# Optimization experiments

Measured on AMD Instinct MI355X. Metric: run time of the kernel, lower is better.

Reference implementation:

```python
import jax, jax.numpy as jnp
import numpy as np

B, N = 32, 1024  # batch, square grid size (Ny == Nx forced by expand_as in the torch module)


def setup_inputs() -> dict:
    key = jax.random.key(0)
    k1, k2, k3 = jax.random.split(key, 3)
    xaxis = jnp.arange(N, dtype=jnp.float32)            # sorted knot positions along x
    yaxis = jnp.arange(N, dtype=jnp.float32)            # sorted knot positions along y
    signal = jax.random.normal(k1, (B, N, N), dtype=jnp.float32)
    # queries constrained to [0.5, N-3] so gathered indices I+1 stay in-bounds for the
    # (N-1)-length slope tensors, matching the valid-domain assumption of the torch code
    xs = jax.random.uniform(k2, (N,), minval=0.5, maxval=float(N - 3), dtype=jnp.float32)
    ys = jax.random.uniform(k3, (N,), minval=0.5, maxval=float(N - 3), dtype=jnp.float32)
    return {"xaxis": xaxis, "yaxis": yaxis, "signal": signal, "xs": xs, "ys": ys}


def _h_poly(t):
    # Cubic Hermite basis: rows of A = [[1,0,-3,2],[0,1,-2,1],[0,0,3,-2],[0,0,-1,1]] dotted with [1,t,t^2,t^3]
    t2 = t * t
    t3 = t2 * t
    h0 = 1.0 - 3.0 * t2 + 2.0 * t3
    h1 = t - 2.0 * t2 + t3
    h2 = 3.0 * t2 - 2.0 * t3
    h3 = t3 - t2
    return h0, h1, h2, h3


def _interp1d(inp, axis1d, m, q):
    # inp: [..., N] values, m: [..., N-1] slopes, axis1d: [N] shared knots, q: [M] queries
    # torch.searchsorted(x0[...,1:-1], xs) with right=False == jnp.searchsorted side='left'
    I = jnp.searchsorted(axis1d[1:-1], q)          # [M], int
    x = axis1d[I]                                  # [M]
    dx = axis1d[I + 1] - x                         # [M]
    t = (q - x) / dx                               # [M]
    h0, h1, h2, h3 = _h_poly(t)

    def g(a, idx):
        idx_b = jnp.broadcast_to(idx, a.shape[:-1] + idx.shape)
        return jnp.take_along_axis(a, idx_b, axis=-1)

    return (h0 * g(inp, I)
            + h1 * g(m, I) * dx
            + h2 * g(inp, I + 1)
            + h3 * g(m, I + 1) * dx)


def reference(xaxis, yaxis, signal, xs, ys):
    # slopes (x1/x2 are just the 1D axes broadcast over signal, so diffs reduce to 1D diffs)
    m1 = (signal[..., 1:] - signal[..., :-1]) / (xaxis[1:] - xaxis[:-1])        # [B,N,N-1]
    sT = jnp.swapaxes(signal, -2, -1)
    m2 = (sT[..., 1:] - sT[..., :-1]) / (yaxis[1:] - yaxis[:-1])                # [B,N,N-1]
    out = jnp.swapaxes(_interp1d(signal, xaxis, m1, xs), -2, -1)                # [B,Mx,N]
    out = jnp.swapaxes(_interp1d(out, yaxis, m2, ys), -2, -1)                   # [B,My,N]
    return out
```

## Files before the change

### kernel.cpp

```cpp
#include <hip/hip_runtime.h>


#define NGRID 1024
#define BATCH 32

__global__ __launch_bounds__(256) void hermite2d_fused(
    const float* __restrict__ signal,
    const float* __restrict__ xs,
    const float* __restrict__ ys,
    float* __restrict__ out)
{
    const int k = blockIdx.x;
    const int b = blockIdx.y;
    const int t = threadIdx.x;

    __shared__ float crow[NGRID];

    const float qy = ys[k];
    int Iy = (int)floorf(qy);
    if (Iy < 0) Iy = 0;
    if (Iy > NGRID - 3) Iy = NGRID - 3;
    const float ty  = qy - (float)Iy;
    const float ty2 = ty * ty;
    const float ty3 = ty2 * ty;
    const float h0y = 1.0f - 3.0f * ty2 + 2.0f * ty3;
    const float h1y = ty - 2.0f * ty2 + ty3;
    const float h2y = 3.0f * ty2 - 2.0f * ty3;
    const float h3y = ty3 - ty2;

    const float4* src4 = (const float4*)(signal + ((size_t)b * NGRID + (size_t)Iy) * NGRID);
    const float4 r0 = src4[t];
    const float4 r1 = src4[t + NGRID / 4];
    const float4 r2 = src4[t + NGRID / 2];

    float4 c;
    c.x = h0y * r0.x + h2y * r1.x;
    c.y = h0y * r0.y + h2y * r1.y;
    c.z = h0y * r0.z + h2y * r1.z;
    c.w = h0y * r0.w + h2y * r1.w;
    ((float4*)crow)[t] = c;

    float colp[4];
    colp[0] = h1y * (r1.x - r0.x) + h3y * (r2.x - r1.x);
    colp[1] = h1y * (r1.y - r0.y) + h3y * (r2.y - r1.y);
    colp[2] = h1y * (r1.z - r0.z) + h3y * (r2.z - r1.z);
    colp[3] = h1y * (r1.w - r0.w) + h3y * (r2.w - r1.w);

    const float4 q4 = ((const float4*)xs)[t];
    const float qx[4] = { q4.x, q4.y, q4.z, q4.w };

    __syncthreads();

    float4 res;
    float* resp = (float*)&res;
    #pragma unroll
    for (int j = 0; j < 4; ++j) {
        const float q = qx[j];
        int Ix = (int)floorf(q);
        if (Ix < 0) Ix = 0;
        if (Ix > NGRID - 3) Ix = NGRID - 3;
        const float tx = q - (float)Ix;
        const float t2 = tx * tx;
        const float t3 = t2 * tx;
        const float w0 = 1.0f - tx - t2 + t3;
        const float w1 = tx + 2.0f * (t2 - t3);
        const float w2 = t3 - t2;
        const float c0 = crow[Ix];
        const float c1 = crow[Ix + 1];
        const float c2 = crow[Ix + 2];
        resp[j] = w0 * c0 + w1 * c1 + w2 * c2 + colp[j];
    }

    float4* orow4 = (float4*)(out + ((size_t)b * NGRID + (size_t)k) * NGRID);
    orow4[t] = res;
}

extern "C" void kernel_launch(void* const* d_in, const int* in_sizes, int n_in,
                              void* d_out, int out_size, void* d_ws, size_t ws_size,
                              hipStream_t stream) {
    const float* signal = (const float*)d_in[2];
    const float* xs     = (const float*)d_in[3];
    const float* ys     = (const float*)d_in[4];
    float* out          = (float*)d_out;

    dim3 grid(NGRID, BATCH);
    hermite2d_fused<<<grid, 256, 0, stream>>>(signal, xs, ys, out);
}
```

Baseline: 238.6 us.

## Process four batches per block with XCD-aware mapping and nontemporal stores

```diff
diff --git a/kernel.cpp b/kernel.cpp
--- a/kernel.cpp
+++ b/kernel.cpp
@@ -3,6 +3,9 @@
 
 #define NGRID 1024
 #define BATCH 32
+#define KB    4
+
+typedef float nfloat4 __attribute__((ext_vector_type(4)));
 
 __global__ __launch_bounds__(256) void hermite2d_fused(
     const float* __restrict__ signal,
@@ -10,11 +13,13 @@
     const float* __restrict__ ys,
     float* __restrict__ out)
 {
-    const int k = blockIdx.x;
-    const int b = blockIdx.y;
-    const int t = threadIdx.x;
+    const unsigned f = blockIdx.x;
+    const int xcd = (int)(f & 7u);
+    const int k   = (int)(f >> 3);
+    const int b0  = xcd * KB;
+    const int t   = threadIdx.x;
 
-    __shared__ float crow[NGRID];
+    __shared__ float crow[KB][NGRID];
 
     const float qy = ys[k];
     int Iy = (int)floorf(qy);
@@ -28,31 +33,34 @@
     const float h2y = 3.0f * ty2 - 2.0f * ty3;
     const float h3y = ty3 - ty2;
 
-    const float4* src4 = (const float4*)(signal + ((size_t)b * NGRID + (size_t)Iy) * NGRID);
-    const float4 r0 = src4[t];
-    const float4 r1 = src4[t + NGRID / 4];
-    const float4 r2 = src4[t + NGRID / 2];
+    float colp[KB][4];
+    #pragma unroll
+    for (int i = 0; i < KB; ++i) {
+        const float4* src4 =
+            (const float4*)(signal + ((size_t)(b0 + i) * NGRID + (size_t)Iy) * NGRID);
+        const float4 r0 = src4[t];
+        const float4 r1 = src4[t + NGRID / 4];
+        const float4 r2 = src4[t + NGRID / 2];
 
-    float4 c;
-    c.x = h0y * r0.x + h2y * r1.x;
-    c.y = h0y * r0.y + h2y * r1.y;
-    c.z = h0y * r0.z + h2y * r1.z;
-    c.w = h0y * r0.w + h2y * r1.w;
-    ((float4*)crow)[t] = c;
+        float4 c;
+        c.x = h0y * r0.x + h2y * r1.x;
+        c.y = h0y * r0.y + h2y * r1.y;
+        c.z = h0y * r0.z + h2y * r1.z;
+        c.w = h0y * r0.w + h2y * r1.w;
+        ((float4*)crow[i])[t] = c;
 
-    float colp[4];
-    colp[0] = h1y * (r1.x - r0.x) + h3y * (r2.x - r1.x);
-    colp[1] = h1y * (r1.y - r0.y) + h3y * (r2.y - r1.y);
-    colp[2] = h1y * (r1.z - r0.z) + h3y * (r2.z - r1.z);
-    colp[3] = h1y * (r1.w - r0.w) + h3y * (r2.w - r1.w);
+        colp[i][0] = h1y * (r1.x - r0.x) + h3y * (r2.x - r1.x);
+        colp[i][1] = h1y * (r1.y - r0.y) + h3y * (r2.y - r1.y);
+        colp[i][2] = h1y * (r1.z - r0.z) + h3y * (r2.z - r1.z);
+        colp[i][3] = h1y * (r1.w - r0.w) + h3y * (r2.w - r1.w);
+    }
 
     const float4 q4 = ((const float4*)xs)[t];
     const float qx[4] = { q4.x, q4.y, q4.z, q4.w };
 
     __syncthreads();
 
-    float4 res;
-    float* resp = (float*)&res;
+    float4 res[KB];
     #pragma unroll
     for (int j = 0; j < 4; ++j) {
         const float q = qx[j];
@@ -65,14 +73,20 @@
         const float w0 = 1.0f - tx - t2 + t3;
         const float w1 = tx + 2.0f * (t2 - t3);
         const float w2 = t3 - t2;
-        const float c0 = crow[Ix];
-        const float c1 = crow[Ix + 1];
-        const float c2 = crow[Ix + 2];
-        resp[j] = w0 * c0 + w1 * c1 + w2 * c2 + colp[j];
+        #pragma unroll
+        for (int i = 0; i < KB; ++i) {
+            const float c0 = crow[i][Ix];
+            const float c1 = crow[i][Ix + 1];
+            const float c2 = crow[i][Ix + 2];
+            ((float*)&res[i])[j] = w0 * c0 + w1 * c1 + w2 * c2 + colp[i][j];
+        }
     }
 
-    float4* orow4 = (float4*)(out + ((size_t)b * NGRID + (size_t)k) * NGRID);
-    orow4[t] = res;
+    #pragma unroll
+    for (int i = 0; i < KB; ++i) {
+        nfloat4* orow4 = (nfloat4*)(out + ((size_t)(b0 + i) * NGRID + (size_t)k) * NGRID);
+        __builtin_nontemporal_store(*(const nfloat4*)&res[i], &orow4[t]);
+    }
 }
 
 extern "C" void kernel_launch(void* const* d_in, const int* in_sizes, int n_in,
@@ -83,6 +97,6 @@
     const float* ys     = (const float*)d_in[4];
     float* out          = (float*)d_out;
 
-    dim3 grid(NGRID, BATCH);
+    dim3 grid(NGRID * (BATCH / KB));
     hermite2d_fused<<<grid, 256, 0, stream>>>(signal, xs, ys, out);
 }
```

Measured after the change: 255.4 us. +7.0%, slower.
